# Optimization experiments

Measured on AMD Instinct MI355X. Metric: run time of the kernel, lower is better.

## Reference

```python
import jax, jax.numpy as jnp
import numpy as np

T = 2048            # context_length
C = 1024            # embedding size
HEAD_QK = 256       # config.head_qk_size
VOCAB = 50257       # config.vocab_size


def setup_inputs() -> dict:
    key = jax.random.key(0)
    k1, k2, k3, k4 = jax.random.split(key, 4)
    x = jax.random.normal(k1, (T, C), dtype=jnp.float32)
    idx = jax.random.randint(k2, (T,), 0, VOCAB, dtype=jnp.int32)
    # Dense kernels (flax Dense stores kernel as [in, out], no bias)
    Wq = jax.random.normal(k3, (C, HEAD_QK), dtype=jnp.float32) / np.sqrt(C)
    Wk = jax.random.normal(k4, (C, HEAD_QK), dtype=jnp.float32) / np.sqrt(C)
    return {"x": x, "idx": idx, "Wq": Wq, "Wk": Wk}


def reference(x, idx, Wq, Wk):
    # q, k: [T, HEAD_QK]
    q = x @ Wq
    k = x @ Wk
    # causal-masked, softmax-free scores: [T, T]
    c = (q @ k.T) * (1.0 / HEAD_QK)
    causal = jnp.tril(jnp.ones((T, T), dtype=bool))
    c = jnp.where(causal, c, 0.0)
    # c @ one_hot(idx, VOCAB) == segment-sum of c's columns by token id
    # out[t, v] = sum_{s : idx[s] == v} c[t, s]   -> [T, VOCAB]
    out = jax.ops.segment_sum(c.T, idx, num_segments=VOCAB).T
    return out
```

## Files before the change

kernel.cpp:

```cpp
#include <hip/hip_runtime.h>

#define T_CTX 2048
#define C_DIM 1024
#define HQK   256
#define NVOC  50257

typedef float nfloat4 __attribute__((ext_vector_type(4)));

__global__ __launch_bounds__(1024) void k_build_first(const int* __restrict__ idx,
                                                      int* __restrict__ first,
                                                      int* __restrict__ vocab_map) {
    __shared__ int sidx[T_CTX];
    __shared__ int skey[4096];
    __shared__ int sval[4096];
    const int tid = threadIdx.x;
    for (int i = tid; i < T_CTX; i += 1024) sidx[i] = idx[i];
    for (int i = tid; i < 4096; i += 1024) { skey[i] = -1; sval[i] = 0x7fffffff; }
    int4* vm4 = reinterpret_cast<int4*>(vocab_map);
    const int4 neg1 = make_int4(-1, -1, -1, -1);
    for (int i = tid; i < 12564; i += 1024) vm4[i] = neg1;
    if (tid == 0) vocab_map[NVOC - 1] = -1;
    __syncthreads();
#pragma unroll
    for (int rep = 0; rep < 2; ++rep) {
        const int s = tid + rep * 1024;
        const int my = sidx[s];
        int h = (int)(((unsigned)my * 2654435761u) >> 16) & 4095;
        while (true) {
            int k = skey[h];
            if (k == my) break;
            if (k == -1) {
                int old = atomicCAS(&skey[h], -1, my);
                if (old == -1 || old == my) break;
            }
            h = (h + 1) & 4095;
        }
        atomicMin(&sval[h], s);
    }
    __syncthreads();
#pragma unroll
    for (int rep = 0; rep < 2; ++rep) {
        const int s = tid + rep * 1024;
        const int my = sidx[s];
        int h = (int)(((unsigned)my * 2654435761u) >> 16) & 4095;
        while (skey[h] != my) h = (h + 1) & 4095;
        const int mp = sval[h];
        first[s] = mp;
        if (mp == s) vocab_map[my] = s;
    }
}

__global__ __launch_bounds__(512) void k_gemm_qk(const float* __restrict__ x,
                                                 const float* __restrict__ Wq,
                                                 const float* __restrict__ Wk,
                                                 float* __restrict__ qbuf,
                                                 float* __restrict__ kT) {
    __shared__ __align__(16) float As[32 * 132];
    __shared__ __align__(16) float Bs[32 * 68];
    const int row0 = blockIdx.x * 128;
    const int col0 = blockIdx.y * 64;
    const bool is_q = (col0 < HQK);
    const float* __restrict__ W = is_q ? Wq : Wk;
    const int wc0 = is_q ? col0 : (col0 - HQK);
    const int tid = threadIdx.x;
    const int tr = (tid >> 4) << 2;
    const int tc = (tid & 15) << 2;
    const int ak = (tid & 7) << 2;
    const int ar0 = tid >> 3;
    const int bk = tid >> 4, bc = (tid & 15) << 2;
    float acc[4][4] = {};
    for (int k0 = 0; k0 < C_DIM; k0 += 32) {
#pragma unroll
        for (int L = 0; L < 2; ++L) {
            const int ar = ar0 + (L << 6);
            float4 a4 = *reinterpret_cast<const float4*>(&x[(size_t)(row0 + ar) * C_DIM + k0 + ak]);
            As[(ak + 0) * 132 + ar] = a4.x; As[(ak + 1) * 132 + ar] = a4.y;
            As[(ak + 2) * 132 + ar] = a4.z; As[(ak + 3) * 132 + ar] = a4.w;
        }
        float4 b4 = *reinterpret_cast<const float4*>(&W[(size_t)(k0 + bk) * HQK + wc0 + bc]);
        *reinterpret_cast<float4*>(&Bs[bk * 68 + bc]) = b4;
        __syncthreads();
#pragma unroll
        for (int kk = 0; kk < 32; ++kk) {
            float4 av = *reinterpret_cast<const float4*>(&As[kk * 132 + tr]);
            float4 bv = *reinterpret_cast<const float4*>(&Bs[kk * 68 + tc]);
            const float a[4] = {av.x, av.y, av.z, av.w};
            const float b[4] = {bv.x, bv.y, bv.z, bv.w};
#pragma unroll
            for (int i = 0; i < 4; ++i)
#pragma unroll
                for (int j = 0; j < 4; ++j) acc[i][j] = fmaf(a[i], b[j], acc[i][j]);
        }
        __syncthreads();
    }
    if (is_q) {
#pragma unroll
        for (int i = 0; i < 4; ++i) {
            float4 o = {acc[i][0], acc[i][1], acc[i][2], acc[i][3]};
            *reinterpret_cast<float4*>(&qbuf[(size_t)(row0 + tr + i) * HQK + col0 + tc]) = o;
        }
    } else {
#pragma unroll
        for (int j = 0; j < 4; ++j) {
            float4 o = {acc[0][j], acc[1][j], acc[2][j], acc[3][j]};
            *reinterpret_cast<float4*>(&kT[(size_t)(wc0 + tc + j) * T_CTX + row0 + tr]) = o;
        }
    }
}

__global__ __launch_bounds__(512) void k_scores_gemm(const float* __restrict__ q,
                                                     const float* __restrict__ kT,
                                                     float* __restrict__ c) {
    const int bt = blockIdx.x, bs = blockIdx.y;
    if (bs > 2 * bt + 1) return;
    __shared__ __align__(16) float As[32 * 132];
    __shared__ __align__(16) float Bs[32 * 68];
    const int row0 = bt * 128;
    const int col0 = bs * 64;
    const int tid = threadIdx.x;
    const int tr = (tid >> 4) << 2;
    const int tc = (tid & 15) << 2;
    const int ak = (tid & 7) << 2;
    const int ar0 = tid >> 3;
    const int bk = tid >> 4, bc = (tid & 15) << 2;
    float acc[4][4] = {};
    for (int k0 = 0; k0 < HQK; k0 += 32) {
#pragma unroll
        for (int L = 0; L < 2; ++L) {
            const int ar = ar0 + (L << 6);
            float4 a4 = *reinterpret_cast<const float4*>(&q[(size_t)(row0 + ar) * HQK + k0 + ak]);
            As[(ak + 0) * 132 + ar] = a4.x; As[(ak + 1) * 132 + ar] = a4.y;
            As[(ak + 2) * 132 + ar] = a4.z; As[(ak + 3) * 132 + ar] = a4.w;
        }
        float4 b4 = *reinterpret_cast<const float4*>(&kT[(size_t)(k0 + bk) * T_CTX + col0 + bc]);
        *reinterpret_cast<float4*>(&Bs[bk * 68 + bc]) = b4;
        __syncthreads();
#pragma unroll
        for (int kk = 0; kk < 32; ++kk) {
            float4 av = *reinterpret_cast<const float4*>(&As[kk * 132 + tr]);
            float4 bv = *reinterpret_cast<const float4*>(&Bs[kk * 68 + tc]);
            const float a[4] = {av.x, av.y, av.z, av.w};
            const float b[4] = {bv.x, bv.y, bv.z, bv.w};
#pragma unroll
            for (int i = 0; i < 4; ++i)
#pragma unroll
                for (int j = 0; j < 4; ++j) acc[i][j] = fmaf(a[i], b[j], acc[i][j]);
        }
        __syncthreads();
    }
    const float scale = 1.0f / 256.0f;
#pragma unroll
    for (int i = 0; i < 4; ++i) {
        float4 o = {acc[i][0] * scale, acc[i][1] * scale, acc[i][2] * scale, acc[i][3] * scale};
        *reinterpret_cast<float4*>(&c[(size_t)(row0 + tr + i) * T_CTX + col0 + tc]) = o;
    }
}

__global__ __launch_bounds__(256) void k_fold_expand(const float* __restrict__ c,
                                                     const int* __restrict__ first,
                                                     const int* __restrict__ vocab_map,
                                                     float* __restrict__ out) {
    __shared__ float rowc[T_CTX];
    const int t = blockIdx.x;
    for (int i = threadIdx.x; i < T_CTX; i += 256) rowc[i] = 0.0f;
    __syncthreads();
    const int nq = (t >> 2) + 1;
    for (int qd = threadIdx.x; qd < nq; qd += 256) {
        const int s0 = qd << 2;
        float4 v = *reinterpret_cast<const float4*>(&c[(size_t)t * T_CTX + s0]);
        int4 f4 = *reinterpret_cast<const int4*>(&first[s0]);
        if (s0 + 3 <= t) {
            atomicAdd(&rowc[f4.x], v.x); atomicAdd(&rowc[f4.y], v.y);
            atomicAdd(&rowc[f4.z], v.z); atomicAdd(&rowc[f4.w], v.w);
        } else {
            atomicAdd(&rowc[f4.x], v.x);
            if (s0 + 1 <= t) atomicAdd(&rowc[f4.y], v.y);
            if (s0 + 2 <= t) atomicAdd(&rowc[f4.z], v.z);
            if (s0 + 3 <= t) atomicAdd(&rowc[f4.w], v.w);
        }
    }
    __syncthreads();
    float* __restrict__ orow = out + (size_t)t * NVOC;
    const int lead = (4 - (t & 3)) & 3;
    if ((int)threadIdx.x < lead) {
        int m = vocab_map[threadIdx.x];
        orow[threadIdx.x] = (m >= 0) ? rowc[m] : 0.0f;
    }
    const int nvec = (NVOC - lead) >> 2;
    for (int i = threadIdx.x; i < nvec; i += 256) {
        const int v = lead + (i << 2);
        int m0 = vocab_map[v + 0], m1 = vocab_map[v + 1];
        int m2 = vocab_map[v + 2], m3 = vocab_map[v + 3];
        nfloat4 o;
        o.x = (m0 >= 0) ? rowc[m0] : 0.0f;
        o.y = (m1 >= 0) ? rowc[m1] : 0.0f;
        o.z = (m2 >= 0) ? rowc[m2] : 0.0f;
        o.w = (m3 >= 0) ? rowc[m3] : 0.0f;
        __builtin_nontemporal_store(o, reinterpret_cast<nfloat4*>(&orow[v]));
    }
    for (int v = lead + (nvec << 2) + threadIdx.x; v < NVOC; v += 256) {
        int m = vocab_map[v];
        orow[v] = (m >= 0) ? rowc[m] : 0.0f;
    }
}

extern "C" void kernel_launch(void* const* d_in, const int* in_sizes, int n_in,
                              void* d_out, int out_size, void* d_ws, size_t ws_size,
                              hipStream_t stream) {
    const float* x   = (const float*)d_in[0];
    const int*   idx = (const int*)d_in[1];
    const float* Wq  = (const float*)d_in[2];
    const float* Wk  = (const float*)d_in[3];
    float* out = (float*)d_out;

    char* ws = (char*)d_ws;
    float* qbuf      = (float*)(ws);
    float* kT        = (float*)(ws + (2u << 20));
    float* c         = (float*)(ws + (4u << 20));
    int*   first     = (int*)(ws + (20u << 20));
    int*   vocab_map = (int*)(ws + (20u << 20) + (16u << 10));

    k_build_first<<<1, 1024, 0, stream>>>(idx, first, vocab_map);
    dim3 gg(16, 8);
    k_gemm_qk<<<gg, 512, 0, stream>>>(x, Wq, Wk, qbuf, kT);
    dim3 gs(16, 32);
    k_scores_gemm<<<gs, 512, 0, stream>>>(qbuf, kT, c);
    k_fold_expand<<<T_CTX, 256, 0, stream>>>(c, first, vocab_map, out);
}
```

Measured before the change: 590.7 us.

## Zero-fill output rows then scatter sparse vocab entries; prefetch GEMM tiles

```diff
diff --git a/kernel.cpp b/kernel.cpp
--- a/kernel.cpp
+++ b/kernel.cpp
@@ -9,17 +9,17 @@
 
 __global__ __launch_bounds__(1024) void k_build_first(const int* __restrict__ idx,
                                                       int* __restrict__ first,
-                                                      int* __restrict__ vocab_map) {
+                                                      int* __restrict__ nnz_g,
+                                                      int* __restrict__ vlist,
+                                                      int* __restrict__ mlist) {
     __shared__ int sidx[T_CTX];
     __shared__ int skey[4096];
     __shared__ int sval[4096];
+    __shared__ int snnz;
     const int tid = threadIdx.x;
     for (int i = tid; i < T_CTX; i += 1024) sidx[i] = idx[i];
     for (int i = tid; i < 4096; i += 1024) { skey[i] = -1; sval[i] = 0x7fffffff; }
-    int4* vm4 = reinterpret_cast<int4*>(vocab_map);
-    const int4 neg1 = make_int4(-1, -1, -1, -1);
-    for (int i = tid; i < 12564; i += 1024) vm4[i] = neg1;
-    if (tid == 0) vocab_map[NVOC - 1] = -1;
+    if (tid == 0) snnz = 0;
     __syncthreads();
 #pragma unroll
     for (int rep = 0; rep < 2; ++rep) {
@@ -46,18 +46,23 @@
         while (skey[h] != my) h = (h + 1) & 4095;
         const int mp = sval[h];
         first[s] = mp;
-        if (mp == s) vocab_map[my] = s;
-    }
-}
-
-__global__ __launch_bounds__(512) void k_gemm_qk(const float* __restrict__ x,
+        if (mp == s) {
+            int p = atomicAdd(&snnz, 1);
+            vlist[p] = my; mlist[p] = s;
+        }
+    }
+    __syncthreads();
+    if (tid == 0) nnz_g[0] = snnz;
+}
+
+__global__ __launch_bounds__(256) void k_gemm_qk(const float* __restrict__ x,
                                                  const float* __restrict__ Wq,
                                                  const float* __restrict__ Wk,
                                                  float* __restrict__ qbuf,
                                                  float* __restrict__ kT) {
-    __shared__ __align__(16) float As[32 * 132];
+    __shared__ __align__(16) float As[32 * 68];
     __shared__ __align__(16) float Bs[32 * 68];
-    const int row0 = blockIdx.x * 128;
+    const int row0 = blockIdx.x * 64;
     const int col0 = blockIdx.y * 64;
     const bool is_q = (col0 < HQK);
     const float* __restrict__ W = is_q ? Wq : Wk;
@@ -65,24 +70,34 @@
     const int tid = threadIdx.x;
     const int tr = (tid >> 4) << 2;
     const int tc = (tid & 15) << 2;
-    const int ak = (tid & 7) << 2;
-    const int ar0 = tid >> 3;
+    const int ar = tid >> 3, ak = (tid & 7) << 2;
     const int bk = tid >> 4, bc = (tid & 15) << 2;
+    float4 pa[2], pb[2];
+#pragma unroll
+    for (int L = 0; L < 2; ++L) {
+        pa[L] = *reinterpret_cast<const float4*>(&x[(size_t)(row0 + ar + 32 * L) * C_DIM + ak]);
+        pb[L] = *reinterpret_cast<const float4*>(&W[(size_t)(bk + 16 * L) * HQK + wc0 + bc]);
+    }
     float acc[4][4] = {};
     for (int k0 = 0; k0 < C_DIM; k0 += 32) {
 #pragma unroll
         for (int L = 0; L < 2; ++L) {
-            const int ar = ar0 + (L << 6);
-            float4 a4 = *reinterpret_cast<const float4*>(&x[(size_t)(row0 + ar) * C_DIM + k0 + ak]);
-            As[(ak + 0) * 132 + ar] = a4.x; As[(ak + 1) * 132 + ar] = a4.y;
-            As[(ak + 2) * 132 + ar] = a4.z; As[(ak + 3) * 132 + ar] = a4.w;
-        }
-        float4 b4 = *reinterpret_cast<const float4*>(&W[(size_t)(k0 + bk) * HQK + wc0 + bc]);
-        *reinterpret_cast<float4*>(&Bs[bk * 68 + bc]) = b4;
-        __syncthreads();
+            const int arL = ar + 32 * L;
+            As[(ak + 0) * 68 + arL] = pa[L].x; As[(ak + 1) * 68 + arL] = pa[L].y;
+            As[(ak + 2) * 68 + arL] = pa[L].z; As[(ak + 3) * 68 + arL] = pa[L].w;
+            *reinterpret_cast<float4*>(&Bs[(bk + 16 * L) * 68 + bc]) = pb[L];
+        }
+        __syncthreads();
+        if (k0 + 32 < C_DIM) {
+#pragma unroll
+            for (int L = 0; L < 2; ++L) {
+                pa[L] = *reinterpret_cast<const float4*>(&x[(size_t)(row0 + ar + 32 * L) * C_DIM + k0 + 32 + ak]);
+                pb[L] = *reinterpret_cast<const float4*>(&W[(size_t)(k0 + 32 + bk + 16 * L) * HQK + wc0 + bc]);
+            }
+        }
 #pragma unroll
         for (int kk = 0; kk < 32; ++kk) {
-            float4 av = *reinterpret_cast<const float4*>(&As[kk * 132 + tr]);
+            float4 av = *reinterpret_cast<const float4*>(&As[kk * 68 + tr]);
             float4 bv = *reinterpret_cast<const float4*>(&Bs[kk * 68 + tc]);
             const float a[4] = {av.x, av.y, av.z, av.w};
             const float b[4] = {bv.x, bv.y, bv.z, bv.w};
@@ -108,36 +123,46 @@
     }
 }
 
-__global__ __launch_bounds__(512) void k_scores_gemm(const float* __restrict__ q,
+__global__ __launch_bounds__(256) void k_scores_gemm(const float* __restrict__ q,
                                                      const float* __restrict__ kT,
                                                      float* __restrict__ c) {
     const int bt = blockIdx.x, bs = blockIdx.y;
-    if (bs > 2 * bt + 1) return;
-    __shared__ __align__(16) float As[32 * 132];
+    if (bs > bt) return;
+    __shared__ __align__(16) float As[32 * 68];
     __shared__ __align__(16) float Bs[32 * 68];
-    const int row0 = bt * 128;
+    const int row0 = bt * 64;
     const int col0 = bs * 64;
     const int tid = threadIdx.x;
     const int tr = (tid >> 4) << 2;
     const int tc = (tid & 15) << 2;
-    const int ak = (tid & 7) << 2;
-    const int ar0 = tid >> 3;
+    const int ar = tid >> 3, ak = (tid & 7) << 2;
     const int bk = tid >> 4, bc = (tid & 15) << 2;
+    float4 pa[2], pb[2];
+#pragma unroll
+    for (int L = 0; L < 2; ++L) {
+        pa[L] = *reinterpret_cast<const float4*>(&q[(size_t)(row0 + ar + 32 * L) * HQK + ak]);
+        pb[L] = *reinterpret_cast<const float4*>(&kT[(size_t)(bk + 16 * L) * T_CTX + col0 + bc]);
+    }
     float acc[4][4] = {};
     for (int k0 = 0; k0 < HQK; k0 += 32) {
 #pragma unroll
         for (int L = 0; L < 2; ++L) {
-            const int ar = ar0 + (L << 6);
-            float4 a4 = *reinterpret_cast<const float4*>(&q[(size_t)(row0 + ar) * HQK + k0 + ak]);
-            As[(ak + 0) * 132 + ar] = a4.x; As[(ak + 1) * 132 + ar] = a4.y;
-            As[(ak + 2) * 132 + ar] = a4.z; As[(ak + 3) * 132 + ar] = a4.w;
-        }
-        float4 b4 = *reinterpret_cast<const float4*>(&kT[(size_t)(k0 + bk) * T_CTX + col0 + bc]);
-        *reinterpret_cast<float4*>(&Bs[bk * 68 + bc]) = b4;
-        __syncthreads();
+            const int arL = ar + 32 * L;
+            As[(ak + 0) * 68 + arL] = pa[L].x; As[(ak + 1) * 68 + arL] = pa[L].y;
+            As[(ak + 2) * 68 + arL] = pa[L].z; As[(ak + 3) * 68 + arL] = pa[L].w;
+            *reinterpret_cast<float4*>(&Bs[(bk + 16 * L) * 68 + bc]) = pb[L];
+        }
+        __syncthreads();
+        if (k0 + 32 < HQK) {
+#pragma unroll
+            for (int L = 0; L < 2; ++L) {
+                pa[L] = *reinterpret_cast<const float4*>(&q[(size_t)(row0 + ar + 32 * L) * HQK + k0 + 32 + ak]);
+                pb[L] = *reinterpret_cast<const float4*>(&kT[(size_t)(k0 + 32 + bk + 16 * L) * T_CTX + col0 + bc]);
+            }
+        }
 #pragma unroll
         for (int kk = 0; kk < 32; ++kk) {
-            float4 av = *reinterpret_cast<const float4*>(&As[kk * 132 + tr]);
+            float4 av = *reinterpret_cast<const float4*>(&As[kk * 68 + tr]);
             float4 bv = *reinterpret_cast<const float4*>(&Bs[kk * 68 + tc]);
             const float a[4] = {av.x, av.y, av.z, av.w};
             const float b[4] = {bv.x, bv.y, bv.z, bv.w};
@@ -158,7 +183,9 @@
 
 __global__ __launch_bounds__(256) void k_fold_expand(const float* __restrict__ c,
                                                      const int* __restrict__ first,
-                                                     const int* __restrict__ vocab_map,
+                                                     const int* __restrict__ nnz_g,
+                                                     const int* __restrict__ vlist,
+                                                     const int* __restrict__ mlist,
                                                      float* __restrict__ out) {
     __shared__ float rowc[T_CTX];
     const int t = blockIdx.x;
@@ -179,28 +206,19 @@
             if (s0 + 3 <= t) atomicAdd(&rowc[f4.w], v.w);
         }
     }
-    __syncthreads();
     float* __restrict__ orow = out + (size_t)t * NVOC;
     const int lead = (4 - (t & 3)) & 3;
-    if ((int)threadIdx.x < lead) {
-        int m = vocab_map[threadIdx.x];
-        orow[threadIdx.x] = (m >= 0) ? rowc[m] : 0.0f;
-    }
+    if ((int)threadIdx.x < lead) orow[threadIdx.x] = 0.0f;
     const int nvec = (NVOC - lead) >> 2;
-    for (int i = threadIdx.x; i < nvec; i += 256) {
-        const int v = lead + (i << 2);
-        int m0 = vocab_map[v + 0], m1 = vocab_map[v + 1];
-        int m2 = vocab_map[v + 2], m3 = vocab_map[v + 3];
-        nfloat4 o;
-        o.x = (m0 >= 0) ? rowc[m0] : 0.0f;
-        o.y = (m1 >= 0) ? rowc[m1] : 0.0f;
-        o.z = (m2 >= 0) ? rowc[m2] : 0.0f;
-        o.w = (m3 >= 0) ? rowc[m3] : 0.0f;
-        __builtin_nontemporal_store(o, reinterpret_cast<nfloat4*>(&orow[v]));
-    }
-    for (int v = lead + (nvec << 2) + threadIdx.x; v < NVOC; v += 256) {
-        int m = vocab_map[v];
-        orow[v] = (m >= 0) ? rowc[m] : 0.0f;
+    const nfloat4 z4 = {0.0f, 0.0f, 0.0f, 0.0f};
+    for (int i = threadIdx.x; i < nvec; i += 256)
+        __builtin_nontemporal_store(z4, reinterpret_cast<nfloat4*>(&orow[lead + (i << 2)]));
+    for (int v = lead + (nvec << 2) + threadIdx.x; v < NVOC; v += 256) orow[v] = 0.0f;
+    __syncthreads();
+    const int nnz = nnz_g[0];
+    for (int i = threadIdx.x; i < nnz; i += 256) {
+        const int m = mlist[i];
+        if (m <= t) orow[vlist[i]] = rowc[m];
     }
 }
 
@@ -214,16 +232,18 @@
     float* out = (float*)d_out;
 
     char* ws = (char*)d_ws;
-    float* qbuf      = (float*)(ws);
-    float* kT        = (float*)(ws + (2u << 20));
-    float* c         = (float*)(ws + (4u << 20));
-    int*   first     = (int*)(ws + (20u << 20));
-    int*   vocab_map = (int*)(ws + (20u << 20) + (16u << 10));
-
-    k_build_first<<<1, 1024, 0, stream>>>(idx, first, vocab_map);
-    dim3 gg(16, 8);
-    k_gemm_qk<<<gg, 512, 0, stream>>>(x, Wq, Wk, qbuf, kT);
-    dim3 gs(16, 32);
-    k_scores_gemm<<<gs, 512, 0, stream>>>(qbuf, kT, c);
-    k_fold_expand<<<T_CTX, 256, 0, stream>>>(c, first, vocab_map, out);
-}
+    float* qbuf   = (float*)(ws);
+    float* kT     = (float*)(ws + (2u << 20));
+    float* c      = (float*)(ws + (4u << 20));
+    int*   first  = (int*)(ws + (20u << 20));
+    int*   nnz_g  = (int*)(ws + (20u << 20) + (16u << 10));
+    int*   vlist  = (int*)(ws + (20u << 20) + (17u << 10));
+    int*   mlist  = (int*)(ws + (20u << 20) + (26u << 10));
+
+    k_build_first<<<1, 1024, 0, stream>>>(idx, first, nnz_g, vlist, mlist);
+    dim3 gg(32, 8);
+    k_gemm_qk<<<gg, 256, 0, stream>>>(x, Wq, Wk, qbuf, kT);
+    dim3 gs(32, 32);
+    k_scores_gemm<<<gs, 256, 0, stream>>>(qbuf, kT, c);
+    k_fold_expand<<<T_CTX, 256, 0, stream>>>(c, first, nnz_g, vlist, mlist, out);
+}
```

Result: slower. 686.9 us (+16.3%).
